# Kernel optimization log

Measured on AMD Instinct MI355X. Metric: run time of the kernel, lower is better.

Reference implementation:

```python
import jax, jax.numpy as jnp
import numpy as np

B, L, D_IN, D_OUT = 8, 2048, 256, 256


def setup_inputs() -> dict:
    key = jax.random.key(0)
    ks = jax.random.split(key, 7)
    s_in = 1.0 / np.sqrt(D_IN)
    return {
        "x": jax.random.normal(ks[0], (B, L, D_IN), dtype=jnp.float32),
        "Wq": jax.random.uniform(ks[1], (D_OUT, D_IN), jnp.float32, -s_in, s_in),
        "bq": jax.random.uniform(ks[2], (D_OUT,), jnp.float32, -s_in, s_in),
        "Wk": jax.random.uniform(ks[3], (D_OUT, D_IN), jnp.float32, -s_in, s_in),
        "bk": jax.random.uniform(ks[4], (D_OUT,), jnp.float32, -s_in, s_in),
        "Wv": jax.random.uniform(ks[5], (D_OUT, D_IN), jnp.float32, -s_in, s_in),
        "bv": jax.random.uniform(ks[6], (D_OUT,), jnp.float32, -s_in, s_in),
    }


def reference(x, Wq, bq, Wk, bk, Wv, bv):
    # QKV projections (torch Linear: y = x @ W.T + b)
    Q = jnp.einsum("bld,od->blo", x, Wq) + bq  # [B, L, D_OUT]
    K = jnp.einsum("bld,od->blo", x, Wk) + bk
    V = jnp.einsum("bld,od->blo", x, Wv) + bv
    scale = jnp.float32(D_OUT) ** 0.5
    E = jnp.einsum("bqd,bkd->bqk", Q, K) / scale  # [B, L, L]
    # NON-STANDARD: softmax over dim=1 (the query axis / columns of E)
    A = jax.nn.softmax(E, axis=1)
    C = jnp.einsum("bqk,bkd->bqd", A, V)  # [B, L, D_OUT]
    S_p = jnp.concatenate([Q, C], axis=1)  # [B, 2L, D_OUT]
    return (S_p, A)
```

## Files before the change

### kernel.cpp

```cpp
#include <hip/hip_runtime.h>
#include <hip/hip_bf16.h>
#include <stdint.h>

#define B_ 8
#define L_ 2048
#define D_ 256

typedef unsigned short u16;
typedef __attribute__((ext_vector_type(4))) float f32x4;
typedef __attribute__((ext_vector_type(8))) short bf16x8;

__device__ __forceinline__ u16 f2b(float f) {
  union { float f; unsigned u; } v; v.f = f;
  unsigned r = v.u + 0x7FFFu + ((v.u >> 16) & 1u);
  return (u16)(r >> 16);
}

__device__ __forceinline__ void comb(float& m, float& s, float m2, float s2) {
  float mn = fmaxf(m, m2);
  s = s * __expf(m - mn) + s2 * __expf(m2 - mn);
  m = mn;
}

__device__ __forceinline__ void async_copy16(const void* g, u16* l) {
  __builtin_amdgcn_global_load_lds(
      (const __attribute__((address_space(1))) unsigned*)g,
      (__attribute__((address_space(3))) unsigned*)l,
      16, 0, 0);
}

template<int KD>
__device__ __forceinline__ void gemm_core(const u16* __restrict__ Ag,
                                          const u16* __restrict__ Bg,
                                          int tile_m, int tile_n,
                                          u16* lds_a, u16* lds_b,
                                          f32x4 acc[4][4]) {
  const int tid  = threadIdx.x;
  const int wave = tid >> 6, lane = tid & 63;
  const int qd = lane >> 4, ln = lane & 15;
  const int wm = wave >> 1, wn = wave & 1;
  const int lrow = lane >> 2;
  const int lcol = (lane & 3) * 8;
  const u16* Abase = Ag + (size_t)tile_m * KD + lcol;
  const u16* Bbase = Bg + (size_t)tile_n * KD + lcol;

  for (int k0 = 0; k0 < KD; k0 += 32) {
#pragma unroll
    for (int j = 0; j < 2; ++j) {
      const int r0 = j * 64 + wave * 16;
      async_copy16(Abase + (size_t)(r0 + lrow) * KD + k0, lds_a + r0 * 32);
      async_copy16(Bbase + (size_t)(r0 + lrow) * KD + k0, lds_b + r0 * 32);
    }
    __syncthreads();
    bf16x8 af[4], bg[4];
#pragma unroll
    for (int i = 0; i < 4; ++i) {
      af[i] = *(const bf16x8*)(lds_a + (wm * 64 + i * 16 + ln) * 32 + qd * 8);
      bg[i] = *(const bf16x8*)(lds_b + (wn * 64 + i * 16 + ln) * 32 + qd * 8);
    }
#pragma unroll
    for (int i = 0; i < 4; ++i)
#pragma unroll
      for (int j = 0; j < 4; ++j)
        acc[i][j] = __builtin_amdgcn_mfma_f32_16x16x32_bf16(af[i], bg[j], acc[i][j], 0, 0, 0);
    __syncthreads();
  }
}

__global__ __launch_bounds__(256) void cvt_kernel(const float* __restrict__ x,
    const float* __restrict__ Wq, const float* __restrict__ Wk, const float* __restrict__ Wv,
    u16* __restrict__ xb, u16* __restrict__ Wb) {
  const int i = blockIdx.x * 256 + threadIdx.x;
  const int NX4 = (B_ * L_ * D_) / 4;
  f32x4 v;
  u16* dst;
  if (i < NX4) {
    v = ((const f32x4*)x)[i];
    dst = xb + (size_t)i * 4;
  } else {
    int wi = i - NX4;
    int z = wi >> 14;
    int off = wi & 16383;
    const float* W = (z == 0) ? Wq : (z == 1 ? Wk : Wv);
    v = ((const f32x4*)W)[off];
    dst = Wb + (size_t)z * 65536 + (size_t)off * 4;
  }
  unsigned p0 = (unsigned)f2b(v.x) | ((unsigned)f2b(v.y) << 16);
  unsigned p1 = (unsigned)f2b(v.z) | ((unsigned)f2b(v.w) << 16);
  *(uint2*)dst = make_uint2(p0, p1);
}

__global__ __launch_bounds__(256) void qkv_gemm(const u16* __restrict__ xb, const u16* __restrict__ Wb,
    const float* __restrict__ bq, const float* __restrict__ bk, const float* __restrict__ bv,
    u16* __restrict__ Qb, u16* __restrict__ Kb, u16* __restrict__ Vb,
    float* __restrict__ out_sp) {
  __shared__ u16 lds_a[128 * 32], lds_b[128 * 32];
  const int z = blockIdx.z;
  const float* bias = (z == 0) ? bq : (z == 1 ? bk : bv);
  u16* dst = (z == 0) ? Qb : (z == 1 ? Kb : Vb);
  const int tile_m = blockIdx.x * 128, tile_n = blockIdx.y * 128;
  f32x4 acc[4][4];
#pragma unroll
  for (int i = 0; i < 4; ++i)
#pragma unroll
    for (int j = 0; j < 4; ++j) acc[i][j] = (f32x4){0.f, 0.f, 0.f, 0.f};
  gemm_core<256>(xb, Wb + (size_t)z * 256 * 256, tile_m, tile_n, lds_a, lds_b, acc);

  const int lane = threadIdx.x & 63, wave = threadIdx.x >> 6;
  const int qd = lane >> 4, ln = lane & 15, wm = wave >> 1, wn = wave & 1;
#pragma unroll
  for (int i = 0; i < 4; ++i)
#pragma unroll
    for (int j = 0; j < 4; ++j) {
      const int col = tile_n + wn * 64 + j * 16 + ln;
      const float bvv = bias[col];
      const int row0 = tile_m + wm * 64 + i * 16 + qd * 4;
#pragma unroll
      for (int r = 0; r < 4; ++r) {
        const int row = row0 + r;
        const float val = acc[i][j][r] + bvv;
        dst[(size_t)row * D_ + col] = f2b(val);
        if (z == 0) {
          const int bb = row >> 11, l = row & 2047;
          out_sp[((size_t)bb * (2 * L_) + l) * D_ + col] = val;
        }
      }
    }
}

__global__ __launch_bounds__(256) void transpose_v(const u16* __restrict__ Vb, u16* __restrict__ Vbt) {
  const int b = blockIdx.z;
  const int l0 = blockIdx.x * 64;
  const int d0 = blockIdx.y * 64;
  __shared__ u16 t[64][65];
  const int tx = threadIdx.x & 63;
  const int ty = threadIdx.x >> 6;
  const u16* src = Vb + (size_t)b * L_ * D_;
  for (int j = ty; j < 64; j += 4)
    t[j][tx] = src[(size_t)(l0 + j) * D_ + d0 + tx];
  __syncthreads();
  u16* dst = Vbt + (size_t)b * D_ * L_;
  for (int j = ty; j < 64; j += 4)
    dst[(size_t)(d0 + j) * L_ + l0 + tx] = t[tx][j];
}

__global__ __launch_bounds__(256) void e_gemm(const u16* __restrict__ Qb, const u16* __restrict__ Kb,
                                              float* __restrict__ Ebuf,
                                              float* __restrict__ pm, float* __restrict__ ps) {
  __shared__ u16 lds_a[128 * 32], lds_b[128 * 32];
  __shared__ float sm_m[4][64], sm_s[4][64];
  const int b = blockIdx.z;
  const int tile_m = blockIdx.x * 128, tile_n = blockIdx.y * 128;
  f32x4 acc[4][4];
#pragma unroll
  for (int i = 0; i < 4; ++i)
#pragma unroll
    for (int j = 0; j < 4; ++j) acc[i][j] = (f32x4){0.f, 0.f, 0.f, 0.f};
  gemm_core<256>(Qb + (size_t)b * L_ * D_, Kb + (size_t)b * L_ * D_, tile_m, tile_n, lds_a, lds_b, acc);

  float* Eb = Ebuf + (size_t)b * L_ * L_;
  const int tid = threadIdx.x;
  const int lane = tid & 63, wave = tid >> 6;
  const int qd = lane >> 4, ln = lane & 15, wm = wave >> 1, wn = wave & 1;
#pragma unroll
  for (int j = 0; j < 4; ++j) {
    const int col = tile_n + wn * 64 + j * 16 + ln;
    const int row0 = tile_m + wm * 64 + qd * 4;
    float m = -1e30f;
#pragma unroll
    for (int i = 0; i < 4; ++i)
#pragma unroll
      for (int r = 0; r < 4; ++r)
        m = fmaxf(m, acc[i][j][r] * 0.0625f);
    float s = 0.f;
#pragma unroll
    for (int i = 0; i < 4; ++i)
#pragma unroll
      for (int r = 0; r < 4; ++r) {
        const float e = acc[i][j][r] * 0.0625f;
        Eb[(size_t)(row0 + i * 16 + r) * L_ + col] = e;
        s += __expf(e - m);
      }
    comb(m, s, __shfl_xor(m, 16), __shfl_xor(s, 16));
    comb(m, s, __shfl_xor(m, 32), __shfl_xor(s, 32));
    if (qd == 0) { sm_m[wave][j * 16 + ln] = m; sm_s[wave][j * 16 + ln] = s; }
  }
  __syncthreads();
  if (tid < 128) {
    const int w = tid >> 6, c = tid & 63;
    float m = sm_m[w][c], s = sm_s[w][c];
    comb(m, s, sm_m[w + 2][c], sm_s[w + 2][c]);
    const size_t idx = (size_t)blockIdx.x * (B_ * L_) + (size_t)b * L_ + tile_n + w * 64 + c;
    pm[idx] = m;
    ps[idx] = s;
  }
}

__global__ __launch_bounds__(256) void stats_reduce(const float* __restrict__ pm,
                                                    const float* __restrict__ ps,
                                                    float* __restrict__ mOut, float* __restrict__ rOut) {
  const int idx = blockIdx.x * 256 + threadIdx.x;
  float m = -1e30f, s = 0.f;
#pragma unroll
  for (int t = 0; t < 16; ++t)
    comb(m, s, pm[t * (B_ * L_) + idx], ps[t * (B_ * L_) + idx]);
  mOut[idx] = m;
  rOut[idx] = 1.0f / s;
}

__global__ __launch_bounds__(256) void apply_kernel(float* __restrict__ EA, u16* __restrict__ Ab,
                                                    const float* __restrict__ mArr,
                                                    const float* __restrict__ rArr) {
  const size_t i4 = (size_t)blockIdx.x * 256 + threadIdx.x;
  const int k4 = (int)(i4 & 511);
  const size_t row = i4 >> 9;
  const int b = (int)(row >> 11);
  f32x4 e = ((const f32x4*)EA)[i4];
  const f32x4 mv = *(const f32x4*)(mArr + (size_t)b * L_ + k4 * 4);
  const f32x4 rv = *(const f32x4*)(rArr + (size_t)b * L_ + k4 * 4);
  f32x4 a;
  a.x = __expf(e.x - mv.x) * rv.x;
  a.y = __expf(e.y - mv.y) * rv.y;
  a.z = __expf(e.z - mv.z) * rv.z;
  a.w = __expf(e.w - mv.w) * rv.w;
  ((f32x4*)EA)[i4] = a;
  unsigned p0 = (unsigned)f2b(a.x) | ((unsigned)f2b(a.y) << 16);
  unsigned p1 = (unsigned)f2b(a.z) | ((unsigned)f2b(a.w) << 16);
  *(uint2*)(Ab + i4 * 4) = make_uint2(p0, p1);
}

__global__ __launch_bounds__(256) void av_gemm(const u16* __restrict__ Ab, const u16* __restrict__ Vbt,
                                               float* __restrict__ out_sp) {
  __shared__ u16 lds_a[128 * 32], lds_b[128 * 32];
  const int b = blockIdx.z;
  const int tile_m = blockIdx.x * 128, tile_n = blockIdx.y * 128;
  f32x4 acc[4][4];
#pragma unroll
  for (int i = 0; i < 4; ++i)
#pragma unroll
    for (int j = 0; j < 4; ++j) acc[i][j] = (f32x4){0.f, 0.f, 0.f, 0.f};
  gemm_core<2048>(Ab + (size_t)b * L_ * L_, Vbt + (size_t)b * D_ * L_, tile_m, tile_n, lds_a, lds_b, acc);

  const int lane = threadIdx.x & 63, wave = threadIdx.x >> 6;
  const int qd = lane >> 4, ln = lane & 15, wm = wave >> 1, wn = wave & 1;
#pragma unroll
  for (int i = 0; i < 4; ++i)
#pragma unroll
    for (int j = 0; j < 4; ++j) {
      const int col = tile_n + wn * 64 + j * 16 + ln;
      const int row0 = tile_m + wm * 64 + i * 16 + qd * 4;
#pragma unroll
      for (int r = 0; r < 4; ++r)
        out_sp[((size_t)b * (2 * L_) + L_ + row0 + r) * D_ + col] = acc[i][j][r];
    }
}

extern "C" void kernel_launch(void* const* d_in, const int* in_sizes, int n_in,
                              void* d_out, int out_size, void* d_ws, size_t ws_size,
                              hipStream_t stream) {
  const float* x  = (const float*)d_in[0];
  const float* Wq = (const float*)d_in[1];
  const float* bq = (const float*)d_in[2];
  const float* Wk = (const float*)d_in[3];
  const float* bk = (const float*)d_in[4];
  const float* Wv = (const float*)d_in[5];
  const float* bv = (const float*)d_in[6];

  float* out    = (float*)d_out;
  float* outA   = out + (size_t)B_ * (2 * L_) * D_;

  u16* w   = (u16*)d_ws;
  u16* xb  = w;
  u16* Wb  = xb + 4194304;
  u16* Qb  = Wb + 196608;
  u16* Kb  = Qb + 4194304;
  u16* Vb  = Kb + 4194304;
  u16* Vbt = Vb + 4194304;
  u16* Ab  = Vbt + 4194304;
  float* mArr = (float*)(Ab + 33554432);
  float* rArr = mArr + B_ * L_;
  float* pm   = rArr + B_ * L_;
  float* ps   = pm + 16 * B_ * L_;

  cvt_kernel<<<4288, 256, 0, stream>>>(x, Wq, Wk, Wv, xb, Wb);
  qkv_gemm<<<dim3(128, 2, 3), 256, 0, stream>>>(xb, Wb, bq, bk, bv, Qb, Kb, Vb, out);
  transpose_v<<<dim3(32, 4, 8), 256, 0, stream>>>(Vb, Vbt);
  e_gemm<<<dim3(16, 16, 8), 256, 0, stream>>>(Qb, Kb, outA, pm, ps);
  stats_reduce<<<64, 256, 0, stream>>>(pm, ps, mArr, rArr);
  apply_kernel<<<32768, 256, 0, stream>>>(outA, Ab, mArr, rArr);
  av_gemm<<<dim3(16, 2, 8), 256, 0, stream>>>(Ab, Vbt, out);
}
```

Before: 337.3 us.

## Store scores in bf16 and fuse softmax normalization into split-K AV GEMM

The score matrix E is now written as bf16 instead of fp32, which halves that write. The separate apply pass is removed. The stats kernel produces a single exp(-m)/s factor per column, and the AV kernel recomputes the normalized A from bf16 E in registers, writes fp32 A once, and feeds bf16 A into MFMA. The AV GEMM now uses split-K with direct global fragment loads and no LDS staging, and a small combine kernel sums the partial C tiles. This removes the full fp32 read-modify-write of A and the bf16 A round trip. In exchange, E is read twice (once per D split), operand reuse through LDS is lost, and A picks up extra error from the bf16-rounded scores before exp.

New measurement: 355.8 us. +5.5%, slower.

```diff
diff --git a/kernel.cpp b/kernel.cpp
--- a/kernel.cpp
+++ b/kernel.cpp
@@ -14,6 +14,11 @@
   union { float f; unsigned u; } v; v.f = f;
   unsigned r = v.u + 0x7FFFu + ((v.u >> 16) & 1u);
   return (u16)(r >> 16);
+}
+
+__device__ __forceinline__ float b2f(u16 u) {
+  union { unsigned u; float f; } v; v.u = ((unsigned)u) << 16;
+  return v.f;
 }
 
 __device__ __forceinline__ void comb(float& m, float& s, float m2, float s2) {
@@ -145,7 +150,7 @@
 }
 
 __global__ __launch_bounds__(256) void e_gemm(const u16* __restrict__ Qb, const u16* __restrict__ Kb,
-                                              float* __restrict__ Ebuf,
+                                              u16* __restrict__ Ebuf,
                                               float* __restrict__ pm, float* __restrict__ ps) {
   __shared__ u16 lds_a[128 * 32], lds_b[128 * 32];
   __shared__ float sm_m[4][64], sm_s[4][64];
@@ -158,7 +163,7 @@
     for (int j = 0; j < 4; ++j) acc[i][j] = (f32x4){0.f, 0.f, 0.f, 0.f};
   gemm_core<256>(Qb + (size_t)b * L_ * D_, Kb + (size_t)b * L_ * D_, tile_m, tile_n, lds_a, lds_b, acc);
 
-  float* Eb = Ebuf + (size_t)b * L_ * L_;
+  u16* Eb = Ebuf + (size_t)b * L_ * L_;
   const int tid = threadIdx.x;
   const int lane = tid & 63, wave = tid >> 6;
   const int qd = lane >> 4, ln = lane & 15, wm = wave >> 1, wn = wave & 1;
@@ -178,7 +183,7 @@
 #pragma unroll
       for (int r = 0; r < 4; ++r) {
         const float e = acc[i][j][r] * 0.0625f;
-        Eb[(size_t)(row0 + i * 16 + r) * L_ + col] = e;
+        Eb[(size_t)(row0 + i * 16 + r) * L_ + col] = f2b(e);
         s += __expf(e - m);
       }
     comb(m, s, __shfl_xor(m, 16), __shfl_xor(s, 16));
@@ -198,61 +203,102 @@
 
 __global__ __launch_bounds__(256) void stats_reduce(const float* __restrict__ pm,
                                                     const float* __restrict__ ps,
-                                                    float* __restrict__ mOut, float* __restrict__ rOut) {
+                                                    float* __restrict__ rrOut) {
   const int idx = blockIdx.x * 256 + threadIdx.x;
   float m = -1e30f, s = 0.f;
 #pragma unroll
   for (int t = 0; t < 16; ++t)
     comb(m, s, pm[t * (B_ * L_) + idx], ps[t * (B_ * L_) + idx]);
-  mOut[idx] = m;
-  rOut[idx] = 1.0f / s;
-}
-
-__global__ __launch_bounds__(256) void apply_kernel(float* __restrict__ EA, u16* __restrict__ Ab,
-                                                    const float* __restrict__ mArr,
-                                                    const float* __restrict__ rArr) {
-  const size_t i4 = (size_t)blockIdx.x * 256 + threadIdx.x;
-  const int k4 = (int)(i4 & 511);
-  const size_t row = i4 >> 9;
-  const int b = (int)(row >> 11);
-  f32x4 e = ((const f32x4*)EA)[i4];
-  const f32x4 mv = *(const f32x4*)(mArr + (size_t)b * L_ + k4 * 4);
-  const f32x4 rv = *(const f32x4*)(rArr + (size_t)b * L_ + k4 * 4);
-  f32x4 a;
-  a.x = __expf(e.x - mv.x) * rv.x;
-  a.y = __expf(e.y - mv.y) * rv.y;
-  a.z = __expf(e.z - mv.z) * rv.z;
-  a.w = __expf(e.w - mv.w) * rv.w;
-  ((f32x4*)EA)[i4] = a;
-  unsigned p0 = (unsigned)f2b(a.x) | ((unsigned)f2b(a.y) << 16);
-  unsigned p1 = (unsigned)f2b(a.z) | ((unsigned)f2b(a.w) << 16);
-  *(uint2*)(Ab + i4 * 4) = make_uint2(p0, p1);
-}
-
-__global__ __launch_bounds__(256) void av_gemm(const u16* __restrict__ Ab, const u16* __restrict__ Vbt,
-                                               float* __restrict__ out_sp) {
-  __shared__ u16 lds_a[128 * 32], lds_b[128 * 32];
+  rrOut[idx] = __expf(-m) / s;
+}
+
+__global__ __launch_bounds__(256) void av_fused(const u16* __restrict__ Eb16,
+                                                const u16* __restrict__ Vbt,
+                                                const float* __restrict__ rr,
+                                                float* __restrict__ Aout,
+                                                float* __restrict__ Cp) {
   const int b = blockIdx.z;
-  const int tile_m = blockIdx.x * 128, tile_n = blockIdx.y * 128;
+  const int tm = blockIdx.x * 128;
+  const int dsplit = blockIdx.y >> 1, ks = blockIdx.y & 1;
+  const int tile_n = dsplit * 128;
+  const int tid = threadIdx.x, wave = tid >> 6, lane = tid & 63;
+  const int qd = lane >> 4, ln = lane & 15, wm = wave >> 1, wn = wave & 1;
+  const u16* Eb = Eb16 + (size_t)b * L_ * L_;
+  const u16* Vt = Vbt + (size_t)b * D_ * L_;
+  const float* rrb = rr + b * L_;
+  float* Ab = Aout + (size_t)b * L_ * L_;
+  const bool wA = (dsplit == 0) && (wn == 0);
+
   f32x4 acc[4][4];
 #pragma unroll
   for (int i = 0; i < 4; ++i)
 #pragma unroll
     for (int j = 0; j < 4; ++j) acc[i][j] = (f32x4){0.f, 0.f, 0.f, 0.f};
-  gemm_core<2048>(Ab + (size_t)b * L_ * L_, Vbt + (size_t)b * D_ * L_, tile_m, tile_n, lds_a, lds_b, acc);
-
-  const int lane = threadIdx.x & 63, wave = threadIdx.x >> 6;
-  const int qd = lane >> 4, ln = lane & 15, wm = wave >> 1, wn = wave & 1;
+
+  const int arow0 = tm + wm * 64 + ln;
+  const int brow0 = tile_n + wn * 64 + ln;
+  const int k_begin = ks * (L_ / 2), k_end = k_begin + (L_ / 2);
+
+  for (int k0 = k_begin; k0 < k_end; k0 += 32) {
+    const int kk = k0 + qd * 8;
+    float rv[8];
+    *(f32x4*)rv       = *(const f32x4*)(rrb + kk);
+    *(f32x4*)(rv + 4) = *(const f32x4*)(rrb + kk + 4);
+    bf16x8 af[4], bg[4];
+#pragma unroll
+    for (int i = 0; i < 4; ++i) {
+      bf16x8 raw = *(const bf16x8*)(Eb + (size_t)(arow0 + i * 16) * L_ + kk);
+      bg[i] = *(const bf16x8*)(Vt + (size_t)(brow0 + i * 16) * L_ + kk);
+      float a[8];
+#pragma unroll
+      for (int e = 0; e < 8; ++e)
+        a[e] = __expf(b2f((u16)raw[e])) * rv[e];
+      if (wA) {
+        float* dst = Ab + (size_t)(arow0 + i * 16) * L_ + kk;
+        *(f32x4*)dst       = (f32x4){a[0], a[1], a[2], a[3]};
+        *(f32x4*)(dst + 4) = (f32x4){a[4], a[5], a[6], a[7]};
+      }
+      bf16x8 t;
+#pragma unroll
+      for (int e = 0; e < 8; ++e) t[e] = (short)f2b(a[e]);
+      af[i] = t;
+    }
+#pragma unroll
+    for (int i = 0; i < 4; ++i)
+#pragma unroll
+      for (int j = 0; j < 4; ++j)
+        acc[i][j] = __builtin_amdgcn_mfma_f32_16x16x32_bf16(af[i], bg[j], acc[i][j], 0, 0, 0);
+  }
+
+  float* cp = Cp + ((((size_t)b * 16 + blockIdx.x) * 2 + dsplit) * 2 + ks) * (128 * 128);
 #pragma unroll
   for (int i = 0; i < 4; ++i)
 #pragma unroll
     for (int j = 0; j < 4; ++j) {
-      const int col = tile_n + wn * 64 + j * 16 + ln;
-      const int row0 = tile_m + wm * 64 + i * 16 + qd * 4;
+      const int row0 = wm * 64 + i * 16 + qd * 4;
+      const int col = wn * 64 + j * 16 + ln;
 #pragma unroll
       for (int r = 0; r < 4; ++r)
-        out_sp[((size_t)b * (2 * L_) + L_ + row0 + r) * D_ + col] = acc[i][j][r];
-    }
+        cp[(size_t)(row0 + r) * 128 + col] = acc[i][j][r];
+    }
+}
+
+__global__ __launch_bounds__(256) void c_combine(const float* __restrict__ Cp,
+                                                 float* __restrict__ out_sp) {
+  const int t = blockIdx.x * 256 + threadIdx.x;
+  const int di4 = t & 31;
+  int x = t >> 5;
+  const int qi = x & 127; x >>= 7;
+  const int ds = x & 1;   x >>= 1;
+  const int tm = x & 15;
+  const int b  = x >> 4;
+  const size_t base = ((((size_t)b * 16 + tm) * 2 + ds) * 2) * (128 * 128)
+                      + (size_t)qi * 128 + di4 * 4;
+  f32x4 va = *(const f32x4*)(Cp + base);
+  f32x4 vb = *(const f32x4*)(Cp + base + 128 * 128);
+  const int q = tm * 128 + qi;
+  const int d = ds * 128 + di4 * 4;
+  *(f32x4*)(out_sp + ((size_t)b * (2 * L_) + L_ + q) * D_ + d) = va + vb;
 }
 
 extern "C" void kernel_launch(void* const* d_in, const int* in_sizes, int n_in,
@@ -266,27 +312,27 @@
   const float* Wv = (const float*)d_in[5];
   const float* bv = (const float*)d_in[6];
 
-  float* out    = (float*)d_out;
-  float* outA   = out + (size_t)B_ * (2 * L_) * D_;
-
-  u16* w   = (u16*)d_ws;
-  u16* xb  = w;
-  u16* Wb  = xb + 4194304;
-  u16* Qb  = Wb + 196608;
-  u16* Kb  = Qb + 4194304;
-  u16* Vb  = Kb + 4194304;
-  u16* Vbt = Vb + 4194304;
-  u16* Ab  = Vbt + 4194304;
-  float* mArr = (float*)(Ab + 33554432);
-  float* rArr = mArr + B_ * L_;
-  float* pm   = rArr + B_ * L_;
-  float* ps   = pm + 16 * B_ * L_;
+  float* out  = (float*)d_out;
+  float* outA = out + (size_t)B_ * (2 * L_) * D_;
+
+  u16* w    = (u16*)d_ws;
+  u16* xb   = w;
+  u16* Wb   = xb + 4194304;
+  u16* Qb   = Wb + 196608;
+  u16* Kb   = Qb + 4194304;
+  u16* Vb   = Kb + 4194304;
+  u16* Vbt  = Vb + 4194304;
+  u16* Eb16 = Vbt + 4194304;
+  float* rrArr = (float*)(Eb16 + 33554432);
+  float* pm    = rrArr + 16384;
+  float* ps    = pm + 262144;
+  float* Cp = (float*)w;
 
   cvt_kernel<<<4288, 256, 0, stream>>>(x, Wq, Wk, Wv, xb, Wb);
   qkv_gemm<<<dim3(128, 2, 3), 256, 0, stream>>>(xb, Wb, bq, bk, bv, Qb, Kb, Vb, out);
   transpose_v<<<dim3(32, 4, 8), 256, 0, stream>>>(Vb, Vbt);
-  e_gemm<<<dim3(16, 16, 8), 256, 0, stream>>>(Qb, Kb, outA, pm, ps);
-  stats_reduce<<<64, 256, 0, stream>>>(pm, ps, mArr, rArr);
-  apply_kernel<<<32768, 256, 0, stream>>>(outA, Ab, mArr, rArr);
-  av_gemm<<<dim3(16, 2, 8), 256, 0, stream>>>(Ab, Vbt, out);
-}
+  e_gemm<<<dim3(16, 16, 8), 256, 0, stream>>>(Qb, Kb, Eb16, pm, ps);
+  stats_reduce<<<64, 256, 0, stream>>>(pm, ps, rrArr);
+  av_fused<<<dim3(16, 4, 8), 256, 0, stream>>>(Eb16, Vbt, rrArr, outA, Cp);
+  c_combine<<<4096, 256, 0, stream>>>(Cp, out);
+}
```
